# Kernel tuning notes

Hardware: AMD Instinct MI355X
Metric: run time of the kernel (lower is better)

The kernel has to match this reference:

```python
import jax, jax.numpy as jnp
import numpy as np

D_MODEL = 256
N_HEADS = 1
N_LEVELS = 4
N_POINTS = 4
NP9 = N_POINTS * 9  # 9-neighborhood around each top-k index


def setup_inputs():
    key = jax.random.key(0)
    k = jax.random.split(key, 4)
    N, Lq = 1, 2048
    H = W = 64
    Lin = N_LEVELS * H * W
    query = jax.random.normal(k[0], (N, Lq, D_MODEL), jnp.float32)
    reference_points = jax.random.uniform(k[1], (N, Lq, N_LEVELS, 2), dtype=jnp.float32)
    input_flatten = jax.random.normal(k[2], (N, Lin, D_MODEL), jnp.float32)
    input_spatial_shapes = jnp.tile(jnp.array([[H, W]], jnp.int32), (N_LEVELS, 1))
    input_level_start_index = jnp.arange(N_LEVELS, dtype=jnp.int32) * (H * W)
    limit = float(np.sqrt(6.0 / (D_MODEL + D_MODEL)))  # xavier_uniform
    out_w = jax.random.uniform(k[3], (D_MODEL, D_MODEL), jnp.float32, -limit, limit)
    out_b = jnp.zeros((D_MODEL,), jnp.float32)
    return dict(query=query, reference_points=reference_points,
                input_flatten=input_flatten,
                input_spatial_shapes=input_spatial_shapes,
                input_level_start_index=input_level_start_index,
                out_w=out_w, out_b=out_b)


def _bilinear_sample(value_l, loc, Hl, Wl):
    # value_l: [N, heads, Hl*Wl, d]; loc: [N, Lq, heads, P, 2] normalized to [0,1]
    # matches torch.grid_sample(mode='bilinear', padding='zeros', align_corners=False)
    N, Lq, heads, P, _ = loc.shape
    x = loc[..., 0] * Wl - 0.5
    y = loc[..., 1] * Hl - 0.5
    x0 = jnp.floor(x)
    y0 = jnp.floor(y)
    wx = (x - x0).transpose(0, 2, 1, 3)[..., None]  # [N,heads,Lq,P,1]
    wy = (y - y0).transpose(0, 2, 1, 3)[..., None]

    def gather(xi, yi):
        valid = (xi >= 0) & (xi <= Wl - 1) & (yi >= 0) & (yi <= Hl - 1)
        xi_c = jnp.clip(xi, 0, Wl - 1).astype(jnp.int32)
        yi_c = jnp.clip(yi, 0, Hl - 1).astype(jnp.int32)
        idx = (yi_c * Wl + xi_c).transpose(0, 2, 1, 3).reshape(N, heads, Lq * P)
        g = jnp.take_along_axis(value_l, idx[..., None], axis=2)
        g = g.reshape(N, heads, Lq, P, -1)
        return g * valid.transpose(0, 2, 1, 3)[..., None].astype(g.dtype)

    v00 = gather(x0, y0)
    v01 = gather(x0 + 1.0, y0)
    v10 = gather(x0, y0 + 1.0)
    v11 = gather(x0 + 1.0, y0 + 1.0)
    return (v00 * (1 - wx) * (1 - wy) + v01 * wx * (1 - wy)
            + v10 * (1 - wx) * wy + v11 * wx * wy)  # [N,heads,Lq,P,d]


def _forward(query, input_flatten, ss, lsi, out_w, out_b):
    N, Lq, _ = query.shape
    _, Lin, dim = input_flatten.shape
    h = int(ss[0, 0]); w = h
    t = Lin // (h * w)
    d_head = dim // N_HEADS
    value = input_flatten.reshape(N, Lin, N_HEADS, d_head).transpose(0, 2, 1, 3)  # [N,heads,Lin,d]
    # correlation + sharpened softmax + top-k index generation
    corr = (jnp.einsum('nqd,nkd->nqk', query, input_flatten) / dim).reshape(N, Lq, t, h * w)
    prob = jax.nn.softmax(10.0 * corr, axis=-1)
    _, idx = jax.lax.top_k(prob, N_POINTS)  # [N,Lq,t,P], descending like torch.topk
    # 9-neighborhood expansion, cat along last dim => offset-major then point
    neigh = jnp.array([-1 - h, -h, 1 - h, -1, 0, 1, -1 + h, h, 1 + h], jnp.int32)
    ridx = (idx[..., None, :] + neigh[None, None, None, :, None]).reshape(N, Lq, t, NP9)
    ridx = jnp.clip(ridx, 0, (h - 1) * (w - 1))  # faithful: max_grid=(h-1)*(w-1)
    rf = ridx.astype(jnp.float32)
    off_w = jnp.floor(rf / h)
    off_h = rf - off_w * h
    offsets = jnp.stack([off_w, off_h], axis=-1)  # [N,Lq,t,NP9,2]
    sampling_offsets = offsets.reshape(N, Lq, N_HEADS, N_LEVELS, NP9, 2)
    ss_j = jnp.asarray(np.asarray(ss))
    normalizer = jnp.stack([ss_j[:, 1], ss_j[:, 0]], -1).astype(jnp.float32)  # [L,2]
    sampling_locations = sampling_offsets / normalizer[None, None, None, :, None, :]
    aw = 1.0 / (N_LEVELS * NP9)  # softmax of all-ones attention weights => uniform
    out = jnp.zeros((N, N_HEADS, Lq, d_head), jnp.float32)
    for l in range(N_LEVELS):
        Hl, Wl = int(ss[l, 0]), int(ss[l, 1])
        s = int(lsi[l])
        v_l = value[:, :, s:s + Hl * Wl, :]
        samp = _bilinear_sample(v_l, sampling_locations[:, :, :, l], Hl, Wl)
        out = out + aw * samp.sum(axis=3)
    out = out.transpose(0, 2, 1, 3).reshape(N, Lq, dim)
    return out @ out_w.T + out_b, sampling_locations


def reference(query, reference_points, input_flatten, input_spatial_shapes,
              input_level_start_index, out_w, out_b):
    assert reference_points.shape[-1] == 2  # 2-d reference branch
    ss = np.asarray(input_spatial_shapes)
    lsi = np.asarray(input_level_start_index)
    return _forward(query, input_flatten, ss, lsi, out_w, out_b)
```

## Files before the change

kernel.cpp:

```cpp
#include <hip/hip_runtime.h>
#include <cstdint>
#include <cstddef>

#define LQ     2048
#define DM     256
#define NKEY   16384
#define NLVL   4
#define LVLN   4096
#define BM     64
#define BN     128
#define KB     16
#define MGRPS  (LQ / BM)
#define CLIPMX 3969
#define QB     8

__device__ __forceinline__ void ins4(float v, int ix, float4& tv, int4& ti) {
  bool c0 = v > tv.x, c1 = v > tv.y, c2 = v > tv.z, c3 = v > tv.w;
  tv.w = c2 ? tv.z : (c3 ? v : tv.w);
  ti.w = c2 ? ti.z : (c3 ? ix : ti.w);
  tv.z = c1 ? tv.y : (c2 ? v : tv.z);
  ti.z = c1 ? ti.y : (c2 ? ix : ti.z);
  tv.y = c0 ? tv.x : (c1 ? v : tv.y);
  ti.y = c0 ? ti.x : (c1 ? ix : ti.y);
  tv.x = c0 ? v : tv.x;
  ti.x = c0 ? ix : ti.x;
}

__device__ __forceinline__ void ins4_tb(float v, int ix, float4& tv, int4& ti) {
  bool c0 = (v > tv.x) || (v == tv.x && ix < ti.x);
  bool c1 = (v > tv.y) || (v == tv.y && ix < ti.y);
  bool c2 = (v > tv.z) || (v == tv.z && ix < ti.z);
  bool c3 = (v > tv.w) || (v == tv.w && ix < ti.w);
  tv.w = c2 ? tv.z : (c3 ? v : tv.w);
  ti.w = c2 ? ti.z : (c3 ? ix : ti.w);
  tv.z = c1 ? tv.y : (c2 ? v : tv.z);
  ti.z = c1 ? ti.y : (c2 ? ix : ti.z);
  tv.y = c0 ? tv.x : (c1 ? v : tv.y);
  ti.y = c0 ? ti.x : (c1 ? ix : ti.y);
  tv.x = c0 ? v : tv.x;
  ti.x = c0 ? ix : ti.x;
}

#define FMA4(accv, s, bv)                  \
  accv.x = fmaf(s, bv.x, accv.x);          \
  accv.y = fmaf(s, bv.y, accv.y);          \
  accv.z = fmaf(s, bv.z, accv.z);          \
  accv.w = fmaf(s, bv.w, accv.w);

#define GLOAD16(ko)                                                          \
    aR0 = *(const float4*)(Aslab + (size_t)(r4)      * DM + (ko) + s4 * 4);  \
    bR0 = *(const float4*)(Bslab + (size_t)(r4)      * DM + (ko) + s4 * 4);  \
    bR1 = *(const float4*)(Bslab + (size_t)(r4 + 64) * DM + (ko) + s4 * 4);

#define LSTORE16(nb_)                                                                \
    As[nb_][s4*4+0][r4]    = aR0.x; As[nb_][s4*4+1][r4]    = aR0.y;                  \
    As[nb_][s4*4+2][r4]    = aR0.z; As[nb_][s4*4+3][r4]    = aR0.w;                  \
    Bs[nb_][s4*4+0][r4]    = bR0.x; Bs[nb_][s4*4+1][r4]    = bR0.y;                  \
    Bs[nb_][s4*4+2][r4]    = bR0.z; Bs[nb_][s4*4+3][r4]    = bR0.w;                  \
    Bs[nb_][s4*4+0][r4+64] = bR1.x; Bs[nb_][s4*4+1][r4+64] = bR1.y;                  \
    Bs[nb_][s4*4+2][r4+64] = bR1.z; Bs[nb_][s4*4+3][r4+64] = bR1.w;

__global__ __launch_bounds__(256, 2) void gemm_qk16(
    const float* __restrict__ Qm, const float* __restrict__ Kb,
    float* __restrict__ C)
{
  const int tid  = threadIdx.x;
  const int mgrp = blockIdx.x;
  const int nb2  = blockIdx.y;
  const int ty = tid >> 4, tx = tid & 15;
  const int r4 = tid >> 2, s4 = tid & 3;

  __shared__ __align__(16) float As[2][KB][BM + 4];
  __shared__ __align__(16) float Bs[2][KB][BN + 4];

  const float* Aslab = Qm + (size_t)mgrp * BM * DM;
  const float* Bslab = Kb + (size_t)nb2 * BN * DM;

  float4 c0l = {0,0,0,0}, c0h = {0,0,0,0};
  float4 c1l = {0,0,0,0}, c1h = {0,0,0,0};
  float4 c2l = {0,0,0,0}, c2h = {0,0,0,0};
  float4 c3l = {0,0,0,0}, c3h = {0,0,0,0};

  float4 aR0, bR0, bR1;

  GLOAD16(0)
  LSTORE16(0)

#pragma unroll 1
  for (int kc = 0; kc < DM / KB; ++kc) {
    __syncthreads();
    if (kc < DM / KB - 1) {
      GLOAD16((kc + 1) * KB)
    }
    const int buf = kc & 1;
#pragma unroll
    for (int k = 0; k < KB; ++k) {
      const float4 av = *(const float4*)&As[buf][k][ty * 4];
      const float4 b0 = *(const float4*)&Bs[buf][k][tx * 4];
      const float4 b1 = *(const float4*)&Bs[buf][k][64 + tx * 4];
      FMA4(c0l, av.x, b0) FMA4(c0h, av.x, b1)
      FMA4(c1l, av.y, b0) FMA4(c1h, av.y, b1)
      FMA4(c2l, av.z, b0) FMA4(c2h, av.z, b1)
      FMA4(c3l, av.w, b0) FMA4(c3h, av.w, b1)
    }
    if (kc < DM / KB - 1) {
      LSTORE16((kc & 1) ^ 1)
    }
  }

  float* Cp = C + (size_t)(mgrp * BM + ty * 4) * LVLN + nb2 * BN + tx * 4;
  *(float4*)(Cp + 0 * LVLN)      = c0l;  *(float4*)(Cp + 0 * LVLN + 64) = c0h;
  *(float4*)(Cp + 1 * LVLN)      = c1l;  *(float4*)(Cp + 1 * LVLN + 64) = c1h;
  *(float4*)(Cp + 2 * LVLN)      = c2l;  *(float4*)(Cp + 2 * LVLN + 64) = c2h;
  *(float4*)(Cp + 3 * LVLN)      = c3l;  *(float4*)(Cp + 3 * LVLN + 64) = c3h;
}

__global__ __launch_bounds__(256) void topk_loc(
    const float* __restrict__ C, const int lvl,
    int* __restrict__ tix, float* __restrict__ sloc)
{
  const int wid  = threadIdx.x >> 6;
  const int lane = threadIdx.x & 63;
  const int q = blockIdx.x * 4 + wid;
  const float* row = C + (size_t)q * LVLN;

  const float4 NEGI = {-3.4e38f, -3.4e38f, -3.4e38f, -3.4e38f};
  const int4   MAXI = {0x7fffffff, 0x7fffffff, 0x7fffffff, 0x7fffffff};
  float4 tv = NEGI;
  int4   ti = MAXI;

#pragma unroll
  for (int it = 0; it < 16; ++it) {
    const int col = it * 256 + lane * 4;
    const float4 v = *(const float4*)(row + col);
    ins4(v.x, col + 0, tv, ti);
    ins4(v.y, col + 1, tv, ti);
    ins4(v.z, col + 2, tv, ti);
    ins4(v.w, col + 3, tv, ti);
  }
#pragma unroll
  for (int d = 1; d < 64; d <<= 1) {
    const float ovx = __shfl_xor(tv.x, d), ovy = __shfl_xor(tv.y, d),
                ovz = __shfl_xor(tv.z, d), ovw = __shfl_xor(tv.w, d);
    const int   oix = __shfl_xor(ti.x, d), oiy = __shfl_xor(ti.y, d),
                oiz = __shfl_xor(ti.z, d), oiw = __shfl_xor(ti.w, d);
    ins4_tb(ovx, oix, tv, ti);
    ins4_tb(ovy, oiy, tv, ti);
    ins4_tb(ovz, oiz, tv, ti);
    ins4_tb(ovw, oiw, tv, ti);
  }

  const int g = q * NLVL + lvl;
  if (lane < 4) {
    const int li = lane == 0 ? ti.x : (lane == 1 ? ti.y : (lane == 2 ? ti.z : ti.w));
    tix[g * 4 + lane] = li;
  }
  if (lane < 36) {
    const int p  = lane & 3, n9 = lane >> 2;
    const int li = p == 0 ? ti.x : (p == 1 ? ti.y : (p == 2 ? ti.z : ti.w));
    const int dy = n9 / 3 - 1, dx = n9 % 3 - 1;
    int r = li + dy * 64 + dx;
    r = r < 0 ? 0 : (r > CLIPMX ? CLIPMX : r);
    sloc[(size_t)g * 72 + lane * 2 + 0] = (float)(r >> 6) * 0.015625f;
    sloc[(size_t)g * 72 + lane * 2 + 1] = (float)(r & 63) * 0.015625f;
  }
}

__global__ void samp_acc(const float* __restrict__ V, const int* __restrict__ tix,
                         float* __restrict__ pre)
{
  const int q = blockIdx.x, d = threadIdx.x;
  const int nei[9] = {-65, -64, -63, -1, 0, 1, 63, 64, 65};
  float acc = 0.f;
#pragma unroll 1
  for (int l = 0; l < NLVL; ++l) {
    const float* Vb = V + (size_t)l * LVLN * DM;
    for (int p = 0; p < 4; ++p) {
      const int p0 = tix[(q * NLVL + l) * 4 + p];
      const int xw = p0 >> 6, yh = p0 & 63;
      if (p0 >= 65 && p0 <= 3904 && yh >= 1 && yh <= 62) {
#pragma unroll
        for (int a = 0; a < 4; ++a) {
          const int y = yh - 2 + a;
          if (y < 0) continue;
          const float wa = (a == 1 || a == 2) ? 2.f : 1.f;
#pragma unroll
          for (int bb = 0; bb < 4; ++bb) {
            const int x = xw - 2 + bb;
            if (x < 0) continue;
            const float wb = (bb == 1 || bb == 2) ? 2.f : 1.f;
            acc = fmaf(wa * wb, Vb[(size_t)(y * 64 + x) * DM + d], acc);
          }
        }
      } else {
#pragma unroll
        for (int n9 = 0; n9 < 9; ++n9) {
          int r = p0 + nei[n9];
          r = r < 0 ? 0 : (r > CLIPMX ? CLIPMX : r);
          const int x = r >> 6, y = r & 63;
          const int b0 = y * 64 + x;
          float s = Vb[(size_t)b0 * DM + d];
          if (x > 0) s += Vb[(size_t)(b0 - 1) * DM + d];
          if (y > 0) {
            s += Vb[(size_t)(b0 - 64) * DM + d];
            if (x > 0) s += Vb[(size_t)(b0 - 65) * DM + d];
          }
          acc += s;
        }
      }
    }
  }
  pre[(size_t)q * DM + d] = acc * (0.25f / 144.f);
}

__global__ void transp_w(const float* __restrict__ W, float* __restrict__ Wt)
{
  __shared__ float t[32][33];
  const int bx = blockIdx.x * 32, by = blockIdx.y * 32;
  t[threadIdx.y][threadIdx.x] = W[(size_t)(by + threadIdx.y) * DM + bx + threadIdx.x];
  __syncthreads();
  Wt[(size_t)(bx + threadIdx.y) * DM + by + threadIdx.x] = t[threadIdx.x][threadIdx.y];
}

__global__ __launch_bounds__(256) void proj_out(
    const float* __restrict__ pre, const float* __restrict__ Wt,
    const float* __restrict__ bias, float* __restrict__ outp)
{
  const int q0 = blockIdx.x * QB;
  const int e = threadIdx.x;
  float acc[QB];
#pragma unroll
  for (int i = 0; i < QB; ++i) acc[i] = 0.f;
#pragma unroll 4
  for (int d = 0; d < DM; ++d) {
    const float w = Wt[(size_t)d * DM + e];
#pragma unroll
    for (int qq = 0; qq < QB; ++qq)
      acc[qq] = fmaf(pre[(size_t)(q0 + qq) * DM + d], w, acc[qq]);
  }
  const float be = bias[e];
#pragma unroll
  for (int qq = 0; qq < QB; ++qq)
    outp[(size_t)(q0 + qq) * DM + e] = acc[qq] + be;
}

extern "C" void kernel_launch(void* const* d_in, const int* in_sizes, int n_in,
                              void* d_out, int out_size, void* d_ws, size_t ws_size,
                              hipStream_t stream)
{
  const float* Q    = (const float*)d_in[0];
  const float* V    = (const float*)d_in[2];
  const float* W    = (const float*)d_in[5];
  const float* bias = (const float*)d_in[6];

  float* outp = (float*)d_out;
  float* sloc = outp + (size_t)LQ * DM;

  char* ws = (char*)d_ws;
  const size_t CORR_B = (size_t)LQ * LVLN * 4;

  float* corr = (float*)ws;
  int*   tix  = (int*)(ws + CORR_B);
  float* pre  = (float*)(ws + CORR_B + 131072);
  float* Wt   = (float*)(ws + CORR_B + 131072 + 2097152);

  for (int l = 0; l < NLVL; ++l) {
    gemm_qk16<<<dim3(MGRPS, LVLN / BN), 256, 0, stream>>>(
        Q, V + (size_t)l * LVLN * DM, corr);
    topk_loc<<<dim3(LQ / 4), 256, 0, stream>>>(corr, l, tix, sloc);
  }
  samp_acc<<<dim3(LQ), 256, 0, stream>>>(V, tix, pre);
  transp_w<<<dim3(8, 8), dim3(32, 32), 0, stream>>>(W, Wt);
  proj_out<<<dim3(LQ / QB), 256, 0, stream>>>(pre, Wt, bias, outp);
}
```

Baseline: 395.0 us.

## Parallelize sampling across levels and points with float4 loads and reduction

Result: faster. 362.7 us (-8.2%).

```diff
diff --git a/kernel.cpp b/kernel.cpp
--- a/kernel.cpp
+++ b/kernel.cpp
@@ -41,6 +41,16 @@
   ti.x = c0 ? ix : ti.x;
 }
 
+__device__ __forceinline__ void fma4v(float4& acc, float s, const float4& v) {
+  acc.x = fmaf(s, v.x, acc.x);
+  acc.y = fmaf(s, v.y, acc.y);
+  acc.z = fmaf(s, v.z, acc.z);
+  acc.w = fmaf(s, v.w, acc.w);
+}
+__device__ __forceinline__ void add4(float4& acc, const float4& v) {
+  acc.x += v.x; acc.y += v.y; acc.z += v.z; acc.w += v.w;
+}
+
 #define FMA4(accv, s, bv)                  \
   accv.x = fmaf(s, bv.x, accv.x);          \
   accv.y = fmaf(s, bv.y, accv.y);          \
@@ -166,51 +176,90 @@
   }
 }
 
-__global__ void samp_acc(const float* __restrict__ V, const int* __restrict__ tix,
-                         float* __restrict__ pre)
-{
-  const int q = blockIdx.x, d = threadIdx.x;
-  const int nei[9] = {-65, -64, -63, -1, 0, 1, 63, 64, 65};
-  float acc = 0.f;
-#pragma unroll 1
-  for (int l = 0; l < NLVL; ++l) {
-    const float* Vb = V + (size_t)l * LVLN * DM;
-    for (int p = 0; p < 4; ++p) {
-      const int p0 = tix[(q * NLVL + l) * 4 + p];
-      const int xw = p0 >> 6, yh = p0 & 63;
-      if (p0 >= 65 && p0 <= 3904 && yh >= 1 && yh <= 62) {
-#pragma unroll
-        for (int a = 0; a < 4; ++a) {
-          const int y = yh - 2 + a;
-          if (y < 0) continue;
-          const float wa = (a == 1 || a == 2) ? 2.f : 1.f;
-#pragma unroll
-          for (int bb = 0; bb < 4; ++bb) {
-            const int x = xw - 2 + bb;
-            if (x < 0) continue;
-            const float wb = (bb == 1 || bb == 2) ? 2.f : 1.f;
-            acc = fmaf(wa * wb, Vb[(size_t)(y * 64 + x) * DM + d], acc);
-          }
-        }
-      } else {
-#pragma unroll
-        for (int n9 = 0; n9 < 9; ++n9) {
-          int r = p0 + nei[n9];
-          r = r < 0 ? 0 : (r > CLIPMX ? CLIPMX : r);
-          const int x = r >> 6, y = r & 63;
-          const int b0 = y * 64 + x;
-          float s = Vb[(size_t)b0 * DM + d];
-          if (x > 0) s += Vb[(size_t)(b0 - 1) * DM + d];
-          if (y > 0) {
-            s += Vb[(size_t)(b0 - 64) * DM + d];
-            if (x > 0) s += Vb[(size_t)(b0 - 65) * DM + d];
-          }
-          acc += s;
+__global__ __launch_bounds__(256) void samp_acc4(
+    const float* __restrict__ V, const int* __restrict__ tix,
+    float* __restrict__ pre4)
+{
+  const int q = blockIdx.x, l = blockIdx.y;
+  const int p = threadIdx.x >> 6, lane = threadIdx.x & 63;
+  const int c0 = lane * 4;
+  const float* Vb = V + (size_t)l * LVLN * DM;
+
+  const int p0 = tix[(q * NLVL + l) * 4 + p];
+  const int xw = p0 >> 6, yh = p0 & 63;
+  float4 acc = {0.f, 0.f, 0.f, 0.f};
+
+  if (p0 >= 65 && p0 <= 3904 && yh >= 1 && yh <= 62) {
+#pragma unroll
+    for (int a = 0; a < 4; ++a) {
+      const int y = yh - 2 + a;
+      if (y < 0) continue;
+      const float wa = (a == 1 || a == 2) ? 2.f : 1.f;
+#pragma unroll
+      for (int bb = 0; bb < 4; ++bb) {
+        const int x = xw - 2 + bb;
+        if (x < 0) continue;
+        const float wb = (bb == 1 || bb == 2) ? 2.f : 1.f;
+        const float4 v = *(const float4*)(Vb + (size_t)(y * 64 + x) * DM + c0);
+        fma4v(acc, wa * wb, v);
+      }
+    }
+  } else {
+    const int nei[9] = {-65, -64, -63, -1, 0, 1, 63, 64, 65};
+#pragma unroll
+    for (int n9 = 0; n9 < 9; ++n9) {
+      int r = p0 + nei[n9];
+      r = r < 0 ? 0 : (r > CLIPMX ? CLIPMX : r);
+      const int x = r >> 6, y = r & 63;
+      const int b0 = y * 64 + x;
+      float4 s = *(const float4*)(Vb + (size_t)b0 * DM + c0);
+      if (x > 0) {
+        const float4 v = *(const float4*)(Vb + (size_t)(b0 - 1) * DM + c0);
+        add4(s, v);
+      }
+      if (y > 0) {
+        const float4 v = *(const float4*)(Vb + (size_t)(b0 - 64) * DM + c0);
+        add4(s, v);
+        if (x > 0) {
+          const float4 u = *(const float4*)(Vb + (size_t)(b0 - 65) * DM + c0);
+          add4(s, u);
         }
       }
-    }
-  }
-  pre[(size_t)q * DM + d] = acc * (0.25f / 144.f);
+      add4(acc, s);
+    }
+  }
+
+  __shared__ __align__(16) float4 red[4][64];
+  red[p][lane] = acc;
+  __syncthreads();
+  if (p == 0) {
+    const float4 a0 = red[0][lane], a1 = red[1][lane];
+    const float4 a2 = red[2][lane], a3 = red[3][lane];
+    float4 s;
+    s.x = (a0.x + a1.x) + (a2.x + a3.x);
+    s.y = (a0.y + a1.y) + (a2.y + a3.y);
+    s.z = (a0.z + a1.z) + (a2.z + a3.z);
+    s.w = (a0.w + a1.w) + (a2.w + a3.w);
+    *(float4*)(pre4 + ((size_t)l * LQ + q) * DM + c0) = s;
+  }
+}
+
+__global__ __launch_bounds__(256) void sum4(
+    const float* __restrict__ pre4, float* __restrict__ pre)
+{
+  const size_t i = (size_t)blockIdx.x * 256 + threadIdx.x;
+  const size_t n = (size_t)LQ * DM / 4;
+  const float4 a = ((const float4*)pre4)[i];
+  const float4 b = ((const float4*)pre4)[i + n];
+  const float4 c = ((const float4*)pre4)[i + 2 * n];
+  const float4 d = ((const float4*)pre4)[i + 3 * n];
+  const float k = 0.25f / 144.f;
+  float4 s;
+  s.x = ((a.x + b.x) + (c.x + d.x)) * k;
+  s.y = ((a.y + b.y) + (c.y + d.y)) * k;
+  s.z = ((a.z + b.z) + (c.z + d.z)) * k;
+  s.w = ((a.w + b.w) + (c.w + d.w)) * k;
+  ((float4*)pre)[i] = s;
 }
 
 __global__ void transp_w(const float* __restrict__ W, float* __restrict__ Wt)
@@ -263,13 +312,15 @@
   int*   tix  = (int*)(ws + CORR_B);
   float* pre  = (float*)(ws + CORR_B + 131072);
   float* Wt   = (float*)(ws + CORR_B + 131072 + 2097152);
+  float* pre4 = corr;
 
   for (int l = 0; l < NLVL; ++l) {
     gemm_qk16<<<dim3(MGRPS, LVLN / BN), 256, 0, stream>>>(
         Q, V + (size_t)l * LVLN * DM, corr);
     topk_loc<<<dim3(LQ / 4), 256, 0, stream>>>(corr, l, tix, sloc);
   }
-  samp_acc<<<dim3(LQ), 256, 0, stream>>>(V, tix, pre);
+  samp_acc4<<<dim3(LQ, NLVL), 256, 0, stream>>>(V, tix, pre4);
+  sum4<<<dim3(LQ * DM / 1024), 256, 0, stream>>>(pre4, pre);
   transp_w<<<dim3(8, 8), dim3(32, 32), 0, stream>>>(W, Wt);
   proj_out<<<dim3(LQ / QB), 256, 0, stream>>>(pre, Wt, bias, outp);
 }
```
